# Performance work log

Hardware: AMD Instinct MI355X
Metric: run time of the kernel (lower is better)

Reference implementation:

```python
import jax, jax.numpy as jnp
import numpy as np

I, L, T, S = 128, 8, 128, 128   # input neurons, topo batches, neurons per batch, fan-in span
BIG = 1e9
EPS = 1e-5


def setup_inputs() -> dict:
    key = jax.random.key(0)
    ks = jax.random.split(key, 7)
    x = jax.random.normal(ks[0], (I,), jnp.float32)
    # per-neuron weights|bias, scaled down for numerical stability of softmax/gelu chain
    W = jax.random.normal(ks[1], (L, T, S + 1), jnp.float32) * 0.05
    mask = (jax.random.uniform(ks[2], (L, T, S)) > 0.5).astype(jnp.float32)  # DAG connectivity
    attn_t = jax.random.normal(ks[3], (L, 3, S, S + 1), jnp.float32) * 0.05      # topo q/k/v (weight|bias)
    attn_n = jax.random.normal(ks[4], (L, T, 3, S, S + 1), jnp.float32) * 0.05   # per-neuron q/k/v
    # additive attention mask: attend only over a neuron's actual inputs
    attn_mask_n = BIG * (1.0 - mask[:, :, :, None] * mask[:, :, None, :])        # (L,T,S,S)
    norm_params = jnp.stack([jnp.ones((L, S)), jnp.zeros((L, S))], 1) \
        + 0.1 * jax.random.normal(ks[5], (L, 2, S), jnp.float32)                 # gamma, beta
    ada = jnp.ones((L, T, 2), jnp.float32) \
        + 0.1 * jax.random.normal(ks[6], (L, T, 2), jnp.float32)                 # gain, amplification
    span_ids = jnp.arange(L * S, dtype=jnp.int32).reshape(L, S)    # gather indices per topo batch
    tb_ids = I + jnp.arange(L * T, dtype=jnp.int32).reshape(L, T)  # scatter indices per topo batch
    return dict(x=x, W=W, mask=mask, attn_t=attn_t, attn_n=attn_n,
                attn_mask_n=attn_mask_n, norm_params=norm_params, ada=ada,
                span_ids=span_ids, tb_ids=tb_ids)


def _attention(qkv, vals, amask):
    # qkv: (3, S, S+1) stacked query/key/value (weight|bias); vals: (S,)
    wq, bq = qkv[0, :, :-1], qkv[0, :, -1]
    wk, bk = qkv[1, :, :-1], qkv[1, :, -1]
    wv, bv = qkv[2, :, :-1], qkv[2, :, -1]
    q = wq @ vals + bq
    k = wk @ vals + bk
    v = wv @ vals + bv
    scores = jnp.outer(q, k) * jax.lax.rsqrt(jnp.float32(vals.shape[0])) - amask
    return jax.nn.softmax(scores) @ v + vals  # residual connection


def _forward(x, W, mask, attn_t, attn_n, attn_mask_n, norm_params, ada, span_ids, tb_ids):
    values = jnp.zeros((I + L * T,), x.dtype).at[jnp.arange(I)].set(x)
    for b in range(L):  # fixed, small topological batch order
        vals = values[span_ids[b]]                                  # gather fan-in span (S,)
        mu = jnp.mean(vals)
        var = jnp.var(vals)
        vals = (vals - mu) * jax.lax.rsqrt(var + EPS)               # topo norm (standardize)
        vals = vals * norm_params[b, 0] + norm_params[b, 1]
        vals = _attention(attn_t[b], vals, 0.0)                     # topo-level self-attention
        # neuron-level self-attention, vmapped over the batch's T neurons -> (T, S)
        vals_n = jax.vmap(_attention, in_axes=(0, None, 0))(attn_n[b], vals, attn_mask_n[b])
        w, bias = W[b, :, :-1], W[b, :, -1]
        aff = jnp.einsum('ts,ts->t', w * mask[b], vals_n) + bias    # masked affine per neuron
        if b == L - 1:
            out = aff                                               # output neurons: identity transform
        else:
            out = jax.nn.gelu(aff * ada[b, :, 0]) * ada[b, :, 1]    # adaptive activation a*sigma(b*x)
        values = values.at[tb_ids[b]].set(out)
    return values[tb_ids[L - 1]]


def reference(x, W, mask, attn_t, attn_n, attn_mask_n, norm_params, ada, span_ids, tb_ids):
    return _forward(x, W, mask, attn_t, attn_n, attn_mask_n, norm_params, ada, span_ids, tb_ids)
```

## Files before the change

### kernel.cpp

```cpp
#include <hip/hip_runtime.h>
#include <math.h>

#define L_DIM 8
#define T_DIM 128
#define S_DIM 128
#define SP1   129
#define SPAD  132
#define BIGF  1000000000.0f
#define EPSF  1e-5f
#define NTHREADS 1024
#define NWAVES 16
#define TCHUNKS 132

template<int CTRL>
__device__ __forceinline__ float dpp_add_part(float x) {
    int r = __builtin_amdgcn_update_dpp(0, __float_as_int(x), CTRL, 0xF, 0xF, false);
    return __int_as_float(r);
}
__device__ __forceinline__ float dpp16Sum15(float x) {
    x += dpp_add_part<0x111>(x);
    x += dpp_add_part<0x112>(x);
    x += dpp_add_part<0x114>(x);
    x += dpp_add_part<0x118>(x);
    return x;
}
__device__ __forceinline__ float dppSum63(float x) {
    x += dpp_add_part<0x111>(x);
    x += dpp_add_part<0x112>(x);
    x += dpp_add_part<0x114>(x);
    x += dpp_add_part<0x118>(x);
    x += dpp_add_part<0x142>(x);
    x += dpp_add_part<0x143>(x);
    return x;
}
__device__ __forceinline__ float lane63(float x) {
    return __int_as_float(__builtin_amdgcn_readlane(__float_as_int(x), 63));
}

__device__ __forceinline__ void wg_bar() {
    asm volatile("s_waitcnt lgkmcnt(0)" ::: "memory");
    __builtin_amdgcn_s_barrier();
    asm volatile("" ::: "memory");
}
__device__ __forceinline__ void wg_bar_vm() {
    asm volatile("s_waitcnt vmcnt(0) lgkmcnt(0)" ::: "memory");
    __builtin_amdgcn_s_barrier();
    asm volatile("" ::: "memory");
}

__device__ __forceinline__ void gld_lds16(const float* g, float* l) {
    __builtin_amdgcn_global_load_lds(
        (const __attribute__((address_space(1))) void*)g,
        (__attribute__((address_space(3))) void*)l,
        16, 0, 0);
}

__device__ __forceinline__ void stage_t_padded(const float* __restrict__ src,
                                               float* __restrict__ lds,
                                               int wid, int lane) {
#pragma unroll
    for (int k = 0; k < 9; ++k) {
        int c = wid + k * NWAVES;
        if (c < TCHUNKS) {
            int s   = c * 64 + lane;
            int row = s / 33;
            int w   = s - row * 33;
            gld_lds16(src + (size_t)row * SP1 + w * 4, lds + c * 256);
        }
    }
}

__device__ __forceinline__ void mv_ldsT(const float* __restrict__ mat,
                                        const float in[8], int li, int r_base,
                                        float* __restrict__ dst) {
#pragma unroll
    for (int p = 0; p < 2; ++p) {
        int r = r_base + p * 4;
        const float* row = mat + r * SPAD;
        float acc = 0.0f;
#pragma unroll
        for (int e = 0; e < 8; ++e) acc = fmaf(row[li * 8 + e], in[e], acc);
        acc = dpp16Sum15(acc);
        if (li == 15) dst[r] = acc + row[128];
    }
}

__device__ __forceinline__ void mv_regs(const float wv[2][8], const float wb[2],
                                        const float in[8], int li, int r_base,
                                        float* __restrict__ dst) {
#pragma unroll
    for (int p = 0; p < 2; ++p) {
        float acc = 0.0f;
#pragma unroll
        for (int e = 0; e < 8; ++e) acc = fmaf(wv[p][e], in[e], acc);
        acc = dpp16Sum15(acc);
        if (li == 15) dst[r_base + p * 4] = acc + wb[p];
    }
}

__device__ __forceinline__ void row_prefetch(const float* __restrict__ mb_,
                                             int li, int r0, int r1,
                                             float arr[2][8], float* b0, float* b1) {
#pragma unroll
    for (int p = 0; p < 2; ++p) {
        int r = p ? r1 : r0;
        const float* row = mb_ + (size_t)r * SP1 + li * 8;
#pragma unroll
        for (int e = 0; e < 8; ++e) arr[p][e] = row[e];
        float bb = mb_[(size_t)r * SP1 + 128];
        if (p) *b1 = bb; else *b0 = bb;
    }
}

template<bool MASKED>
__device__ __forceinline__ void attn_sm(int li, int r_base,
                                        const float* __restrict__ lds_q,
                                        const float* __restrict__ lds_k,
                                        const float* __restrict__ lds_v,
                                        const float m1mj[8], float mr0, float mr1,
                                        const float* __restrict__ resid,
                                        float* __restrict__ lds_out)
{
    const float scale = 0.08838834764831845f;
    float kx[8], vx[8];
#pragma unroll
    for (int e = 0; e < 8; ++e) { kx[e] = lds_k[li * 8 + e]; vx[e] = lds_v[li * 8 + e]; }
#pragma unroll
    for (int p = 0; p < 2; ++p) {
        int r = r_base + p * 4;
        float qs = lds_q[r] * scale;
        float bp = MASKED ? (BIGF * (p ? mr1 : mr0)) : 0.0f;
        float den = 0.0f, num = 0.0f;
#pragma unroll
        for (int e = 0; e < 8; ++e) {
            float s_ = MASKED ? fmaf(-bp, m1mj[e], qs * kx[e]) : (qs * kx[e]);
            float ee = __expf(s_);
            den += ee;
            num = fmaf(ee, vx[e], num);
        }
        den = dpp16Sum15(den);
        num = dpp16Sum15(num);
        if (li == 15) lds_out[r] = num / den + resid[r];
    }
}

__global__ __launch_bounds__(NTHREADS, 4)
void net_kernel(const float* __restrict__ x,
                const float* __restrict__ W,
                const float* __restrict__ maskp,
                const float* __restrict__ attn_t,
                const float* __restrict__ attn_n,
                const float* __restrict__ norm_params,
                const float* __restrict__ ada,
                float* __restrict__ out,
                unsigned long long* __restrict__ mbox)
{
    const int t    = blockIdx.x;
    const int tid  = threadIdx.x;
    const int lane = tid & 63;
    const int wid  = tid >> 6;
    const int li   = lane & 15;
    const int g    = lane >> 4;
    const int r0   = wid * 8 + g;
    const int r1   = r0 + 4;

    __shared__ float lds_t[2 * S_DIM * SPAD];
    __shared__ float lds_vw[NWAVES * S_DIM];
    __shared__ float lds_q[S_DIM], lds_k[S_DIM], lds_v[S_DIM];
    __shared__ float lds_tv[S_DIM];
    __shared__ float lds_vn[S_DIM];

    float nq[2][8], nk[2][8], nv[2][8];
    float nqb0, nqb1, nkb0, nkb1, nvb0, nvb1;

    {
        const float* srcn = attn_n + (size_t)t * 3 * S_DIM * SP1;
        stage_t_padded(attn_t, lds_t, wid, lane);
        row_prefetch(srcn,                   li, r0, r1, nq, &nqb0, &nqb1);
        row_prefetch(srcn + 1 * S_DIM * SP1, li, r0, r1, nk, &nkb0, &nkb1);
        row_prefetch(srcn + 2 * S_DIM * SP1, li, r0, r1, nv, &nvb0, &nvb1);
    }

    float* vw = lds_vw + wid * S_DIM;

    for (int b = 0; b < L_DIM; ++b) {
        wg_bar_vm();

        float tvw[2][8], tvb0, tvb1;
        row_prefetch(attn_t + ((size_t)b * 3 + 2) * S_DIM * SP1, li, r0, r1,
                     tvw, &tvb0, &tvb1);
        const float* mrow = maskp + (size_t)(b * T_DIM + t) * S_DIM;
        float m1mj[8];
#pragma unroll
        for (int e = 0; e < 8; ++e) m1mj[e] = 1.0f - mrow[li * 8 + e];
        float mr0 = mrow[r0], mr1 = mrow[r1];

        float w0r = 0.f, w1r = 0.f, wb = 0.f, mm0 = 0.f, mm1 = 0.f;
        if (wid == 0) {
            const float* wrow = W + (size_t)(b * T_DIM + t) * SP1;
            w0r = wrow[lane]; w1r = wrow[lane + 64]; wb = wrow[128];
            mm0 = mrow[lane]; mm1 = mrow[lane + 64];
        }

        {
            float np00 = norm_params[(b * 2 + 0) * S_DIM + lane];
            float np10 = norm_params[(b * 2 + 0) * S_DIM + lane + 64];
            float np01 = norm_params[(b * 2 + 1) * S_DIM + lane];
            float np11 = norm_params[(b * 2 + 1) * S_DIM + lane + 64];
            float v0, v1;
            if (b == 0) {
                v0 = x[lane]; v1 = x[lane + 64];
            } else {
                float a00 = ada[((b - 1) * T_DIM + lane) * 2 + 0];
                float a01 = ada[((b - 1) * T_DIM + lane) * 2 + 1];
                float a10 = ada[((b - 1) * T_DIM + lane + 64) * 2 + 0];
                float a11 = ada[((b - 1) * T_DIM + lane + 64) * 2 + 1];
                const unsigned long long* mb_ = mbox + (size_t)(b - 1) * T_DIM;
                unsigned long long u0, u1;
                do { u0 = __hip_atomic_load(&mb_[lane], __ATOMIC_RELAXED, __HIP_MEMORY_SCOPE_AGENT); }
                while ((unsigned int)(u0 >> 32) != (unsigned int)b);
                do { u1 = __hip_atomic_load(&mb_[lane + 64], __ATOMIC_RELAXED, __HIP_MEMORY_SCOPE_AGENT); }
                while ((unsigned int)(u1 >> 32) != (unsigned int)b);
                {
                    float z = __uint_as_float((unsigned int)u0) * a00;
                    float z3 = z * z * z;
                    v0 = 0.5f * z * (1.0f + tanhf(0.7978845608028654f * (z + 0.044715f * z3))) * a01;
                }
                {
                    float z = __uint_as_float((unsigned int)u1) * a10;
                    float z3 = z * z * z;
                    v1 = 0.5f * z * (1.0f + tanhf(0.7978845608028654f * (z + 0.044715f * z3))) * a11;
                }
            }
            float s  = dppSum63(v0 + v1);
            float mu = lane63(s) * (1.0f / 128.0f);
            float d0 = v0 - mu, d1 = v1 - mu;
            float s2 = dppSum63(fmaf(d0, d0, d1 * d1));
            float rstd = rsqrtf(lane63(s2) * (1.0f / 128.0f) + EPSF);
            vw[lane]      = d0 * rstd * np00 + np01;
            vw[lane + 64] = d1 * rstd * np10 + np11;
        }

        {
            float iv[8];
#pragma unroll
            for (int e = 0; e < 8; ++e) iv[e] = vw[li * 8 + e];
            mv_ldsT(lds_t,                iv, li, r0, lds_q);
            mv_ldsT(lds_t + S_DIM * SPAD, iv, li, r0, lds_k);
            float tb[2] = { tvb0, tvb1 };
            mv_regs(tvw, tb, iv, li, r0, lds_v);
        }
        wg_bar();

        if (b < L_DIM - 1)
            stage_t_padded(attn_t + (size_t)(b + 1) * 3 * S_DIM * SP1, lds_t, wid, lane);

        attn_sm<false>(li, r0, lds_q, lds_k, lds_v, m1mj, 0.f, 0.f, vw, lds_tv);
        wg_bar();

        {
            float tvv[8];
#pragma unroll
            for (int e = 0; e < 8; ++e) tvv[e] = lds_tv[li * 8 + e];
            float bq[2] = { nqb0, nqb1 }, bk[2] = { nkb0, nkb1 }, bv[2] = { nvb0, nvb1 };
            mv_regs(nq, bq, tvv, li, r0, lds_q);
            mv_regs(nk, bk, tvv, li, r0, lds_k);
            mv_regs(nv, bv, tvv, li, r0, lds_v);
        }

        if (b < L_DIM - 1) {
            const float* srcn = attn_n + (size_t)((b + 1) * T_DIM + t) * 3 * S_DIM * SP1;
            row_prefetch(srcn,                   li, r0, r1, nq, &nqb0, &nqb1);
            row_prefetch(srcn + 1 * S_DIM * SP1, li, r0, r1, nk, &nkb0, &nkb1);
            row_prefetch(srcn + 2 * S_DIM * SP1, li, r0, r1, nv, &nvb0, &nvb1);
        }
        wg_bar();

        attn_sm<true>(li, r0, lds_q, lds_k, lds_v, m1mj, mr0, mr1, lds_tv, lds_vn);
        wg_bar();

        if (wid == 0) {
            float term = w0r * mm0 * lds_vn[lane] + w1r * mm1 * lds_vn[lane + 64];
            float s = dppSum63(term);
            if (lane == 63) {
                float aff = s + wb;
                if (b == L_DIM - 1) {
                    out[t] = aff;
                } else {
                    unsigned long long u =
                        ((unsigned long long)(unsigned int)(b + 1) << 32) |
                        (unsigned long long)__float_as_uint(aff);
                    __hip_atomic_store(&mbox[(size_t)b * T_DIM + t], u,
                                       __ATOMIC_RELAXED, __HIP_MEMORY_SCOPE_AGENT);
                }
            }
        }
    }
}

extern "C" void kernel_launch(void* const* d_in, const int* in_sizes, int n_in,
                              void* d_out, int out_size, void* d_ws, size_t ws_size,
                              hipStream_t stream) {
    const float* x           = (const float*)d_in[0];
    const float* W           = (const float*)d_in[1];
    const float* maskp       = (const float*)d_in[2];
    const float* attn_t      = (const float*)d_in[3];
    const float* attn_n      = (const float*)d_in[4];
    const float* norm_params = (const float*)d_in[6];
    const float* ada         = (const float*)d_in[7];
    float* out = (float*)d_out;

    unsigned long long* mbox = (unsigned long long*)d_ws;

    hipMemsetAsync(d_ws, 0, (size_t)(L_DIM - 1) * T_DIM * sizeof(unsigned long long), stream);

    void* args[] = { (void*)&x, (void*)&W, (void*)&maskp, (void*)&attn_t, (void*)&attn_n,
                     (void*)&norm_params, (void*)&ada, (void*)&out, (void*)&mbox };
    hipLaunchCooperativeKernel((const void*)net_kernel, dim3(T_DIM), dim3(NTHREADS),
                               args, 0, stream);
}
```

Measured before the change: 494.8 us.

## Stage per-neuron q/k in LDS, read topo weights from global, fuse affine into attention

Swaps what goes into LDS. The per-block neuron-level q/k matrices are now staged in LDS via async global-to-LDS loads, and the shared topo attention weights are read straight from global (cached in L2) during the topo matvec. The masked neuron attention now computes the weighted affine partial sums per wave and reduces them through a small LDS array. This removes one barrier and the lds_vn round trip, and cuts register pressure from holding nq/nk rows. In exchange the topo matvec now issues uncached-in-LDS global reads on the critical path, and the launch_bounds occupancy hint is dropped.

```diff
diff --git a/kernel.cpp b/kernel.cpp
--- a/kernel.cpp
+++ b/kernel.cpp
@@ -10,7 +10,7 @@
 #define EPSF  1e-5f
 #define NTHREADS 1024
 #define NWAVES 16
-#define TCHUNKS 132
+#define NCHUNKS 132
 
 template<int CTRL>
 __device__ __forceinline__ float dpp_add_part(float x) {
@@ -55,13 +55,13 @@
         16, 0, 0);
 }
 
-__device__ __forceinline__ void stage_t_padded(const float* __restrict__ src,
-                                               float* __restrict__ lds,
-                                               int wid, int lane) {
+__device__ __forceinline__ void stage_nqk(const float* __restrict__ src,
+                                          float* __restrict__ lds,
+                                          int wid, int lane) {
 #pragma unroll
     for (int k = 0; k < 9; ++k) {
         int c = wid + k * NWAVES;
-        if (c < TCHUNKS) {
+        if (c < NCHUNKS) {
             int s   = c * 64 + lane;
             int row = s / 33;
             int w   = s - row * 33;
@@ -70,9 +70,24 @@
     }
 }
 
-__device__ __forceinline__ void mv_ldsT(const float* __restrict__ mat,
-                                        const float in[8], int li, int r_base,
-                                        float* __restrict__ dst) {
+__device__ __forceinline__ void mv_glb(const float* __restrict__ mat,
+                                       const float in[8], int li, int r_base,
+                                       float* __restrict__ dst) {
+#pragma unroll
+    for (int p = 0; p < 2; ++p) {
+        int r = r_base + p * 4;
+        const float* row = mat + (size_t)r * SP1;
+        float acc = 0.0f;
+#pragma unroll
+        for (int e = 0; e < 8; ++e) acc = fmaf(row[li * 8 + e], in[e], acc);
+        acc = dpp16Sum15(acc);
+        if (li == 15) dst[r] = acc + row[128];
+    }
+}
+
+__device__ __forceinline__ void mv_stage(const float* __restrict__ mat,
+                                         const float in[8], int li, int r_base,
+                                         float* __restrict__ dst) {
 #pragma unroll
     for (int p = 0; p < 2; ++p) {
         int r = r_base + p * 4;
@@ -112,14 +127,12 @@
     }
 }
 
-template<bool MASKED>
-__device__ __forceinline__ void attn_sm(int li, int r_base,
-                                        const float* __restrict__ lds_q,
-                                        const float* __restrict__ lds_k,
-                                        const float* __restrict__ lds_v,
-                                        const float m1mj[8], float mr0, float mr1,
-                                        const float* __restrict__ resid,
-                                        float* __restrict__ lds_out)
+__device__ __forceinline__ void attn_sm_t(int li, int r_base,
+                                          const float* __restrict__ lds_q,
+                                          const float* __restrict__ lds_k,
+                                          const float* __restrict__ lds_v,
+                                          const float* __restrict__ resid,
+                                          float* __restrict__ lds_out)
 {
     const float scale = 0.08838834764831845f;
     float kx[8], vx[8];
@@ -129,12 +142,10 @@
     for (int p = 0; p < 2; ++p) {
         int r = r_base + p * 4;
         float qs = lds_q[r] * scale;
-        float bp = MASKED ? (BIGF * (p ? mr1 : mr0)) : 0.0f;
         float den = 0.0f, num = 0.0f;
 #pragma unroll
         for (int e = 0; e < 8; ++e) {
-            float s_ = MASKED ? fmaf(-bp, m1mj[e], qs * kx[e]) : (qs * kx[e]);
-            float ee = __expf(s_);
+            float ee = __expf(qs * kx[e]);
             den += ee;
             num = fmaf(ee, vx[e], num);
         }
@@ -144,7 +155,7 @@
     }
 }
 
-__global__ __launch_bounds__(NTHREADS, 4)
+__global__ __launch_bounds__(NTHREADS)
 void net_kernel(const float* __restrict__ x,
                 const float* __restrict__ W,
                 const float* __restrict__ maskp,
@@ -164,43 +175,32 @@
     const int r0   = wid * 8 + g;
     const int r1   = r0 + 4;
 
-    __shared__ float lds_t[2 * S_DIM * SPAD];
+    __shared__ float lds_nqk[2 * S_DIM * SPAD];
     __shared__ float lds_vw[NWAVES * S_DIM];
     __shared__ float lds_q[S_DIM], lds_k[S_DIM], lds_v[S_DIM];
     __shared__ float lds_tv[S_DIM];
-    __shared__ float lds_vn[S_DIM];
-
-    float nq[2][8], nk[2][8], nv[2][8];
-    float nqb0, nqb1, nkb0, nkb1, nvb0, nvb1;
+    __shared__ float lds_aff[NWAVES];
+
+    float nv[2][8];
+    float nvb0, nvb1;
 
     {
         const float* srcn = attn_n + (size_t)t * 3 * S_DIM * SP1;
-        stage_t_padded(attn_t, lds_t, wid, lane);
-        row_prefetch(srcn,                   li, r0, r1, nq, &nqb0, &nqb1);
-        row_prefetch(srcn + 1 * S_DIM * SP1, li, r0, r1, nk, &nkb0, &nkb1);
+        stage_nqk(srcn, lds_nqk, wid, lane);
         row_prefetch(srcn + 2 * S_DIM * SP1, li, r0, r1, nv, &nvb0, &nvb1);
     }
 
     float* vw = lds_vw + wid * S_DIM;
 
     for (int b = 0; b < L_DIM; ++b) {
-        wg_bar_vm();
-
-        float tvw[2][8], tvb0, tvb1;
-        row_prefetch(attn_t + ((size_t)b * 3 + 2) * S_DIM * SP1, li, r0, r1,
-                     tvw, &tvb0, &tvb1);
         const float* mrow = maskp + (size_t)(b * T_DIM + t) * S_DIM;
+        const float* wrow = W + (size_t)(b * T_DIM + t) * SP1;
         float m1mj[8];
 #pragma unroll
         for (int e = 0; e < 8; ++e) m1mj[e] = 1.0f - mrow[li * 8 + e];
         float mr0 = mrow[r0], mr1 = mrow[r1];
-
-        float w0r = 0.f, w1r = 0.f, wb = 0.f, mm0 = 0.f, mm1 = 0.f;
-        if (wid == 0) {
-            const float* wrow = W + (size_t)(b * T_DIM + t) * SP1;
-            w0r = wrow[lane]; w1r = wrow[lane + 64]; wb = wrow[128];
-            mm0 = mrow[lane]; mm1 = mrow[lane + 64];
-        }
+        float wr0 = wrow[r0], wr1 = wrow[r1];
+        float wb  = (wid == 0) ? wrow[128] : 0.0f;
 
         {
             float np00 = norm_params[(b * 2 + 0) * S_DIM + lane];
@@ -245,45 +245,68 @@
             float iv[8];
 #pragma unroll
             for (int e = 0; e < 8; ++e) iv[e] = vw[li * 8 + e];
-            mv_ldsT(lds_t,                iv, li, r0, lds_q);
-            mv_ldsT(lds_t + S_DIM * SPAD, iv, li, r0, lds_k);
-            float tb[2] = { tvb0, tvb1 };
-            mv_regs(tvw, tb, iv, li, r0, lds_v);
+            const float* bb = attn_t + (size_t)b * 3 * S_DIM * SP1;
+            mv_glb(bb,                    iv, li, r0, lds_q);
+            mv_glb(bb + 1 * S_DIM * SP1,  iv, li, r0, lds_k);
+            mv_glb(bb + 2 * S_DIM * SP1,  iv, li, r0, lds_v);
         }
         wg_bar();
 
-        if (b < L_DIM - 1)
-            stage_t_padded(attn_t + (size_t)(b + 1) * 3 * S_DIM * SP1, lds_t, wid, lane);
-
-        attn_sm<false>(li, r0, lds_q, lds_k, lds_v, m1mj, 0.f, 0.f, vw, lds_tv);
-        wg_bar();
+        attn_sm_t(li, r0, lds_q, lds_k, lds_v, vw, lds_tv);
+        wg_bar_vm();
 
         {
             float tvv[8];
 #pragma unroll
             for (int e = 0; e < 8; ++e) tvv[e] = lds_tv[li * 8 + e];
-            float bq[2] = { nqb0, nqb1 }, bk[2] = { nkb0, nkb1 }, bv[2] = { nvb0, nvb1 };
-            mv_regs(nq, bq, tvv, li, r0, lds_q);
-            mv_regs(nk, bk, tvv, li, r0, lds_k);
+            mv_stage(lds_nqk,                 tvv, li, r0, lds_q);
+            mv_stage(lds_nqk + S_DIM * SPAD,  tvv, li, r0, lds_k);
+            float bv[2] = { nvb0, nvb1 };
             mv_regs(nv, bv, tvv, li, r0, lds_v);
         }
+        wg_bar();
 
         if (b < L_DIM - 1) {
             const float* srcn = attn_n + (size_t)((b + 1) * T_DIM + t) * 3 * S_DIM * SP1;
-            row_prefetch(srcn,                   li, r0, r1, nq, &nqb0, &nqb1);
-            row_prefetch(srcn + 1 * S_DIM * SP1, li, r0, r1, nk, &nkb0, &nkb1);
+            stage_nqk(srcn, lds_nqk, wid, lane);
             row_prefetch(srcn + 2 * S_DIM * SP1, li, r0, r1, nv, &nvb0, &nvb1);
         }
+
+        {
+            const float scale = 0.08838834764831845f;
+            float kx[8], vx[8];
+#pragma unroll
+            for (int e = 0; e < 8; ++e) { kx[e] = lds_k[li * 8 + e]; vx[e] = lds_v[li * 8 + e]; }
+            float o0 = 0.0f, o1 = 0.0f;
+#pragma unroll
+            for (int p = 0; p < 2; ++p) {
+                int r = r0 + p * 4;
+                float qs = lds_q[r] * scale;
+                float bp = BIGF * (p ? mr1 : mr0);
+                float den = 0.0f, num = 0.0f;
+#pragma unroll
+                for (int e = 0; e < 8; ++e) {
+                    float s_ = fmaf(-bp, m1mj[e], qs * kx[e]);
+                    float ee = __expf(s_);
+                    den += ee;
+                    num = fmaf(ee, vx[e], num);
+                }
+                den = dpp16Sum15(den);
+                num = dpp16Sum15(num);
+                float o = num / den + lds_tv[r];
+                if (p) o1 = o; else o0 = o;
+            }
+            float part = (li == 15) ? (wr0 * mr0 * o0 + wr1 * mr1 * o1) : 0.0f;
+            part = dppSum63(part);
+            if (lane == 63) lds_aff[wid] = part;
+        }
         wg_bar();
 
-        attn_sm<true>(li, r0, lds_q, lds_k, lds_v, m1mj, mr0, mr1, lds_tv, lds_vn);
-        wg_bar();
-
         if (wid == 0) {
-            float term = w0r * mm0 * lds_vn[lane] + w1r * mm1 * lds_vn[lane + 64];
-            float s = dppSum63(term);
+            float pa = (lane < NWAVES) ? lds_aff[lane] : 0.0f;
+            pa = dppSum63(pa);
             if (lane == 63) {
-                float aff = s + wb;
+                float aff = pa + wb;
                 if (b == L_DIM - 1) {
                     out[t] = aff;
                 } else {
```

After: 427.3 us. 13.6% less time.
